# Kernel tuning notes

Measured on AMD Instinct MI355X. Metric: run time of the kernel, lower is better.

The kernel has to match this reference:

```python
import jax, jax.numpy as jnp
import numpy as np

C = 32        # channels after first 1x1 conv
HEADS = 4     # FuncSelfAttention heads ('channel' head split -> d = C // HEADS)


def setup_inputs() -> dict:
    key = jax.random.key(0)
    ks = jax.random.split(key, 8)
    B, H, W = 8, 512, 512
    s = 0.1
    return {
        "x": jax.random.normal(ks[0], (B, 1, H, W), jnp.float32),
        "n": 8,
        "m": 8,
        # Conv2d(1, C, kernel_size=1) == per-pixel linear 1->C
        "w1": jax.random.normal(ks[1], (C, 1), jnp.float32) * s,
        "b1": jax.random.normal(ks[2], (C,), jnp.float32) * s,
        # fused QKV projection over channels, bias=False
        "wqkv": jax.random.normal(ks[3], (3 * C, C), jnp.float32) * s,
        # output projection of the attention
        "wproj": jax.random.normal(ks[4], (C, C), jnp.float32) * s,
        "bproj": jax.random.normal(ks[5], (C,), jnp.float32) * s,
        # Conv2d(C, 1, kernel_size=1)
        "w2": jax.random.normal(ks[6], (1, C), jnp.float32) * s,
        "b2": jax.random.normal(ks[7], (1,), jnp.float32) * s,
    }


def reference(x, n, m, w1, b1, wqkv, wproj, bproj, w2, b2):
    B, _, H, W = x.shape
    d = C // HEADS
    hh, ww = H // n, W // m
    S, P = n * m, hh * ww  # subdomain tokens, quadrature points per token

    # 1x1 conv (pointwise linear over channel dim)
    h = jnp.einsum('oi,bihw->bohw', w1, x) + b1[None, :, None, None]

    # decompose2d: [B,C,H,W] -> [B, n*m, C, hh, ww] (flatten spatial per token)
    u = h.reshape(B, C, n, hh, m, ww).transpose(0, 2, 4, 1, 3, 5)
    u = u.reshape(B, S, C, P)

    # channel self-attention over subdomain functions
    qkv = jnp.einsum('oc,bscp->bsop', wqkv, u)          # [B,S,3C,P]
    q, k, v = jnp.split(qkv, 3, axis=2)
    q = q.reshape(B, S, HEADS, d, P)
    k = k.reshape(B, S, HEADS, d, P)
    v = v.reshape(B, S, HEADS, d, P)

    # L2 (quadrature-mean) inner product over points + head channels
    scale = 1.0 / (P * np.sqrt(d).astype(np.float32))
    scores = jnp.einsum('bihdp,bjhdp->bhij', q, k) * scale  # [B,H,S,S]
    attn = jax.nn.softmax(scores, axis=-1)
    o = jnp.einsum('bhij,bjhdp->bihdp', attn, v).reshape(B, S, C, P)
    o = jnp.einsum('oc,bscp->bsop', wproj, o) + bproj[None, None, :, None]

    # recompose2d: [B, n*m, C, hh, ww] -> [B, C, H, W]
    o = o.reshape(B, n, m, C, hh, ww).transpose(0, 3, 1, 4, 2, 5)
    o = o.reshape(B, C, H, W)

    # final 1x1 conv C -> 1
    out = jnp.einsum('oc,bchw->bohw', w2, o) + b2[None, :, None, None]
    return out
```

## Files before the change

### kernel.cpp

```cpp
#include <hip/hip_runtime.h>


#define CONST_OFF 0
#define SXP_OFF   16
#define W_OFF     (16 + 128*64)
#define PART_OFF  (W_OFF + 8*4096)

typedef __attribute__((ext_vector_type(8))) short bf16x8;
typedef __attribute__((ext_vector_type(4))) float f32x4;

__device__ __forceinline__ unsigned short f2bf(float f) {
    unsigned int u = __float_as_uint(f);
    u = (u + 0x7FFFu + ((u >> 16) & 1u)) >> 16;
    return (unsigned short)u;
}

__global__ __launch_bounds__(256) void k1_gram(const float* __restrict__ x,
                                               float* __restrict__ ws)
{
    __shared__ unsigned short xsb[64 * 272];
    int b = blockIdx.x >> 4, prg = blockIdx.x & 15;
    int t = threadIdx.x;
    const float* xb = x + (size_t)b * 262144;

    #pragma unroll
    for (int prl = 0; prl < 4; ++prl) {
        int pr = prg * 4 + prl;
        #pragma unroll
        for (int k = 0; k < 4; ++k) {
            int q = t + 256 * k;
            int tj = q >> 7, col4 = q & 127;
            float4 v = *(const float4*)(xb + (tj * 64 + pr) * 512 + col4 * 4);
            int token = tj * 8 + (col4 >> 4);
            ushort4 h;
            h.x = f2bf(v.x); h.y = f2bf(v.y); h.z = f2bf(v.z); h.w = f2bf(v.w);
            *(ushort4*)(&xsb[token * 272 + prl * 64 + (col4 & 15) * 4]) = h;
        }
    }
    __syncthreads();

    if (t < 64) {
        const uint4* p = (const uint4*)(&xsb[t * 272]);
        float s = 0.f;
        #pragma unroll
        for (int c = 0; c < 32; ++c) {
            uint4 u = p[c];
            s += __uint_as_float(u.x << 16) + __uint_as_float(u.x & 0xFFFF0000u)
               + __uint_as_float(u.y << 16) + __uint_as_float(u.y & 0xFFFF0000u)
               + __uint_as_float(u.z << 16) + __uint_as_float(u.z & 0xFFFF0000u)
               + __uint_as_float(u.w << 16) + __uint_as_float(u.w & 0xFFFF0000u);
        }
        ws[SXP_OFF + blockIdx.x * 64 + t] = s;
    }

    int w = t >> 6, lane = t & 63;
    int m = lane & 15, quad = lane >> 4;
    f32x4 acc[4];
    #pragma unroll
    for (int jq = 0; jq < 4; ++jq) acc[jq] = (f32x4){0.f, 0.f, 0.f, 0.f};

    #pragma unroll
    for (int s = 0; s < 8; ++s) {
        int kb = s * 32 + quad * 8;
        bf16x8 a = *(const bf16x8*)(&xsb[(w * 16 + m) * 272 + kb]);
        #pragma unroll
        for (int jq = 0; jq < 4; ++jq) {
            bf16x8 bb = *(const bf16x8*)(&xsb[(jq * 16 + m) * 272 + kb]);
            acc[jq] = __builtin_amdgcn_mfma_f32_16x16x32_bf16(a, bb, acc[jq],
                                                              0, 0, 0);
        }
    }

    float* part = ws + PART_OFF + (size_t)blockIdx.x * 4096;
    #pragma unroll
    for (int jq = 0; jq < 4; ++jq)
        #pragma unroll
        for (int r = 0; r < 4; ++r)
            part[(w * 16 + quad * 4 + r) * 64 + jq * 16 + m] = acc[jq][r];
}

__global__ __launch_bounds__(1024) void k2_attn(
    const float* __restrict__ w1, const float* __restrict__ b1,
    const float* __restrict__ wqkv, const float* __restrict__ wproj,
    const float* __restrict__ bproj, const float* __restrict__ w2,
    const float* __restrict__ b2, float* __restrict__ ws)
{
    __shared__ float arow[96], crow[96], pvec[32];
    __shared__ float cst[16];
    __shared__ float G_s[64 * 65];
    __shared__ float sxp_s[16][64];
    __shared__ float sx_s[64];
    __shared__ float coef_s[4][64];
    __shared__ float m_s[4][64];
    int b = blockIdx.x, t = threadIdx.x;

    if (t < 96) {
        float sa = 0.f, sc = 0.f;
        for (int c = 0; c < 32; ++c) {
            float w = wqkv[t * 32 + c];
            sa += w * w1[c];
            sc += w * b1[c];
        }
        arow[t] = sa; crow[t] = sc;
    } else if (t < 128) {
        int c = t - 96;
        float s = 0.f;
        for (int oc = 0; oc < 32; ++oc) s += w2[oc] * wproj[oc * 32 + c];
        pvec[c] = s;
    }

    {
        const float* p0 = ws + PART_OFF + (size_t)(b * 16) * 4096 + t;
        float a0 = 0.f, a1 = 0.f, a2 = 0.f, a3 = 0.f;
        #pragma unroll
        for (int r = 0; r < 16; ++r) {
            const float* pr = p0 + (size_t)r * 4096;
            a0 += pr[0]; a1 += pr[1024]; a2 += pr[2048]; a3 += pr[3072];
        }
        int e0 = t;
        G_s[(e0 >> 6) * 65 + (e0 & 63)] = a0;
        int e1 = t + 1024;
        G_s[(e1 >> 6) * 65 + (e1 & 63)] = a1;
        int e2 = t + 2048;
        G_s[(e2 >> 6) * 65 + (e2 & 63)] = a2;
        int e3 = t + 3072;
        G_s[(e3 >> 6) * 65 + (e3 & 63)] = a3;
    }

    {
        int j = t & 63, rg = t >> 6;
        sxp_s[rg][j] = ws[SXP_OFF + (b * 16 + rg) * 64 + j];
    }
    __syncthreads();
    if (t < 64) {
        float s = 0.f;
        #pragma unroll
        for (int r = 0; r < 16; ++r) s += sxp_s[r][t];
        sx_s[t] = s;
    }

    const float scale = 1.0f / (4096.0f * 2.8284271247461903f);
    if (t >= 64 && t < 68) {
        int h = t - 64;
        float A = 0.f, Bk = 0.f, g = 0.f;
        #pragma unroll
        for (int dd = 0; dd < 8; ++dd) {
            int o = h * 8 + dd;
            A  += arow[o] * arow[32 + o];
            Bk += crow[o] * arow[32 + o];
            g  += pvec[o] * arow[64 + o];
        }
        cst[h]     = A * scale;
        cst[4 + h] = Bk * scale;
        cst[8 + h] = g;
    } else if (t == 68) {
        float c0 = b2[0];
        for (int c = 0; c < 32; ++c)  c0 += pvec[c] * crow[64 + c];
        for (int oc = 0; oc < 32; ++oc) c0 += w2[oc] * bproj[oc];
        cst[12] = c0;
    }
    __syncthreads();

    if (t < 256) {
        int h = t >> 6, i = t & 63;
        float A  = cst[h];
        float Bk = cst[4 + h];
        float g  = cst[8 + h];
        float m = -1e30f;
        for (int j = 0; j < 64; ++j) {
            float s = A * G_s[i * 65 + j] + Bk * sx_s[j];
            m = fmaxf(m, s);
        }
        float Z = 0.f;
        for (int j = 0; j < 64; ++j) {
            float s = A * G_s[i * 65 + j] + Bk * sx_s[j];
            Z += __expf(s - m);
        }
        coef_s[h][i] = g / Z;
        m_s[h][i]    = m;
    }
    __syncthreads();

    {
        float A0 = cst[0], A1 = cst[1], A2 = cst[2], A3 = cst[3];
        float B0 = cst[4], B1 = cst[5], B2 = cst[6], B3 = cst[7];
        #pragma unroll
        for (int k = 0; k < 4; ++k) {
            int e = t + 1024 * k;
            int i = e >> 6, j = e & 63;
            float G  = G_s[i * 65 + j];
            float sx = sx_s[j];
            float w =
                coef_s[0][i] * __expf(A0 * G + B0 * sx - m_s[0][i]) +
                coef_s[1][i] * __expf(A1 * G + B1 * sx - m_s[1][i]) +
                coef_s[2][i] * __expf(A2 * G + B2 * sx - m_s[2][i]) +
                coef_s[3][i] * __expf(A3 * G + B3 * sx - m_s[3][i]);
            ws[W_OFF + b * 4096 + e] = w;
        }
    }
    if (b == 0 && t == 0) ws[CONST_OFF + 12] = cst[12];
}

__global__ __launch_bounds__(256) void k3_apply(const float* __restrict__ x,
                                                const float* __restrict__ ws,
                                                float* __restrict__ out)
{
    __shared__ unsigned short xt[64 * 72];
    __shared__ unsigned short wsm[64 * 72];
    int b = blockIdx.x >> 6, pr = blockIdx.x & 63;
    int t = threadIdx.x;
    const float* xb = x + (size_t)b * 262144;

    #pragma unroll
    for (int k = 0; k < 4; ++k) {
        int q = t + 256 * k;
        int j = q >> 4, c4 = q & 15;
        int ti = j >> 3, tk = j & 7;
        float4 v = *(const float4*)(xb + (ti * 64 + pr) * 512 + tk * 64 + c4 * 4);
        xt[(4 * c4 + 0) * 72 + j] = f2bf(v.x);
        xt[(4 * c4 + 1) * 72 + j] = f2bf(v.y);
        xt[(4 * c4 + 2) * 72 + j] = f2bf(v.z);
        xt[(4 * c4 + 3) * 72 + j] = f2bf(v.w);
        int i = q >> 4, j4 = q & 15;
        float4 wv = *(const float4*)(ws + W_OFF + b * 4096 + q * 4);
        ushort4 h;
        h.x = f2bf(wv.x); h.y = f2bf(wv.y); h.z = f2bf(wv.z); h.w = f2bf(wv.w);
        *(ushort4*)(&wsm[i * 72 + j4 * 4]) = h;
    }
    __syncthreads();

    int w = t >> 6, lane = t & 63;
    int m = lane & 15, quad = lane >> 4;
    f32x4 acc[4];
    #pragma unroll
    for (int jq = 0; jq < 4; ++jq) acc[jq] = (f32x4){0.f, 0.f, 0.f, 0.f};

    #pragma unroll
    for (int s = 0; s < 2; ++s) {
        int kb = s * 32 + quad * 8;
        bf16x8 a = *(const bf16x8*)(&wsm[(w * 16 + m) * 72 + kb]);
        #pragma unroll
        for (int jq = 0; jq < 4; ++jq) {
            bf16x8 bv = *(const bf16x8*)(&xt[(jq * 16 + m) * 72 + kb]);
            acc[jq] = __builtin_amdgcn_mfma_f32_16x16x32_bf16(a, bv, acc[jq],
                                                              0, 0, 0);
        }
    }

    float c0 = ws[CONST_OFF + 12];
    float* ob = out + (size_t)b * 262144;
    #pragma unroll
    for (int jq = 0; jq < 4; ++jq)
        #pragma unroll
        for (int r = 0; r < 4; ++r) {
            int i = w * 16 + quad * 4 + r;
            int c = jq * 16 + m;
            int ti = i >> 3, tk = i & 7;
            ob[(ti * 64 + pr) * 512 + tk * 64 + c] = acc[jq][r] + c0;
        }
}

extern "C" void kernel_launch(void* const* d_in, const int* in_sizes, int n_in,
                              void* d_out, int out_size, void* d_ws, size_t ws_size,
                              hipStream_t stream) {
    const float* x     = (const float*)d_in[0];
    const float* w1    = (const float*)d_in[3];
    const float* b1    = (const float*)d_in[4];
    const float* wqkv  = (const float*)d_in[5];
    const float* wproj = (const float*)d_in[6];
    const float* bproj = (const float*)d_in[7];
    const float* w2    = (const float*)d_in[8];
    const float* b2    = (const float*)d_in[9];
    float* out = (float*)d_out;
    float* ws  = (float*)d_ws;

    k1_gram<<<128, 256, 0, stream>>>(x, ws);
    k2_attn<<<8, 1024, 0, stream>>>(w1, b1, wqkv, wproj, bproj, w2, b2, ws);
    k3_apply<<<512, 256, 0, stream>>>(x, ws, out);
}
```

Measured before the change: 90.67 us.

## Split attention kernel across row groups and store mixing weights as bf16

The attention kernel now runs 64 blocks of 256 threads instead of 8 blocks of 1024. Each block reduces and processes only 8 rows of the 64x64 Gram matrix for one batch, which spreads the work over more compute units. Each block still recomputes the small weight-derived constants redundantly. The mixing-weight matrix is converted to bf16 inside the attention kernel, halving that workspace traffic, and the apply kernel loads it directly with 16-byte copies instead of converting from fp32.

```diff
diff --git a/kernel.cpp b/kernel.cpp
--- a/kernel.cpp
+++ b/kernel.cpp
@@ -3,8 +3,8 @@
 
 #define CONST_OFF 0
 #define SXP_OFF   16
-#define W_OFF     (16 + 128*64)
-#define PART_OFF  (W_OFF + 8*4096)
+#define WB_OFF    (16 + 128*64)
+#define PART_OFF  (WB_OFF + 8*2048)
 
 typedef __attribute__((ext_vector_type(8))) short bf16x8;
 typedef __attribute__((ext_vector_type(4))) float f32x4;
@@ -79,7 +79,7 @@
             part[(w * 16 + quad * 4 + r) * 64 + jq * 16 + m] = acc[jq][r];
 }
 
-__global__ __launch_bounds__(1024) void k2_attn(
+__global__ __launch_bounds__(256) void k2_attn(
     const float* __restrict__ w1, const float* __restrict__ b1,
     const float* __restrict__ wqkv, const float* __restrict__ wproj,
     const float* __restrict__ bproj, const float* __restrict__ w2,
@@ -87,12 +87,13 @@
 {
     __shared__ float arow[96], crow[96], pvec[32];
     __shared__ float cst[16];
-    __shared__ float G_s[64 * 65];
-    __shared__ float sxp_s[16][64];
+    __shared__ float G_s[8 * 65];
+    __shared__ float sxp_s[4][64];
     __shared__ float sx_s[64];
-    __shared__ float coef_s[4][64];
-    __shared__ float m_s[4][64];
-    int b = blockIdx.x, t = threadIdx.x;
+    __shared__ float coef_s[4][8];
+    __shared__ float m_s[4][8];
+    int b = blockIdx.x >> 3, rg = blockIdx.x & 7;
+    int t = threadIdx.x;
 
     if (t < 96) {
         float sa = 0.f, sc = 0.f;
@@ -110,34 +111,28 @@
     }
 
     {
-        const float* p0 = ws + PART_OFF + (size_t)(b * 16) * 4096 + t;
-        float a0 = 0.f, a1 = 0.f, a2 = 0.f, a3 = 0.f;
+        const float* p0 = ws + PART_OFF + (size_t)(b * 16) * 4096 + rg * 512;
+        float a0 = 0.f, a1 = 0.f;
         #pragma unroll
         for (int r = 0; r < 16; ++r) {
             const float* pr = p0 + (size_t)r * 4096;
-            a0 += pr[0]; a1 += pr[1024]; a2 += pr[2048]; a3 += pr[3072];
-        }
-        int e0 = t;
-        G_s[(e0 >> 6) * 65 + (e0 & 63)] = a0;
-        int e1 = t + 1024;
-        G_s[(e1 >> 6) * 65 + (e1 & 63)] = a1;
-        int e2 = t + 2048;
-        G_s[(e2 >> 6) * 65 + (e2 & 63)] = a2;
-        int e3 = t + 3072;
-        G_s[(e3 >> 6) * 65 + (e3 & 63)] = a3;
-    }
-
-    {
-        int j = t & 63, rg = t >> 6;
-        sxp_s[rg][j] = ws[SXP_OFF + (b * 16 + rg) * 64 + j];
-    }
-    __syncthreads();
-    if (t < 64) {
+            a0 += pr[t]; a1 += pr[t + 256];
+        }
+        int e0 = t;          G_s[(e0 >> 6) * 65 + (e0 & 63)] = a0;
+        int e1 = t + 256;    G_s[(e1 >> 6) * 65 + (e1 & 63)] = a1;
+    }
+
+    {
+        int j = t & 63, r4 = t >> 6;
         float s = 0.f;
         #pragma unroll
-        for (int r = 0; r < 16; ++r) s += sxp_s[r][t];
-        sx_s[t] = s;
-    }
+        for (int k = 0; k < 4; ++k)
+            s += ws[SXP_OFF + (b * 16 + r4 * 4 + k) * 64 + j];
+        sxp_s[r4][j] = s;
+    }
+    __syncthreads();
+    if (t < 64)
+        sx_s[t] = sxp_s[0][t] + sxp_s[1][t] + sxp_s[2][t] + sxp_s[3][t];
 
     const float scale = 1.0f / (4096.0f * 2.8284271247461903f);
     if (t >= 64 && t < 68) {
@@ -161,44 +156,46 @@
     }
     __syncthreads();
 
-    if (t < 256) {
-        int h = t >> 6, i = t & 63;
+    if (t < 32) {
+        int h = t >> 3, il = t & 7;
         float A  = cst[h];
         float Bk = cst[4 + h];
         float g  = cst[8 + h];
         float m = -1e30f;
         for (int j = 0; j < 64; ++j) {
-            float s = A * G_s[i * 65 + j] + Bk * sx_s[j];
+            float s = A * G_s[il * 65 + j] + Bk * sx_s[j];
             m = fmaxf(m, s);
         }
         float Z = 0.f;
         for (int j = 0; j < 64; ++j) {
-            float s = A * G_s[i * 65 + j] + Bk * sx_s[j];
+            float s = A * G_s[il * 65 + j] + Bk * sx_s[j];
             Z += __expf(s - m);
         }
-        coef_s[h][i] = g / Z;
-        m_s[h][i]    = m;
+        coef_s[h][il] = g / Z;
+        m_s[h][il]    = m;
     }
     __syncthreads();
 
     {
         float A0 = cst[0], A1 = cst[1], A2 = cst[2], A3 = cst[3];
         float B0 = cst[4], B1 = cst[5], B2 = cst[6], B3 = cst[7];
-        #pragma unroll
-        for (int k = 0; k < 4; ++k) {
-            int e = t + 1024 * k;
-            int i = e >> 6, j = e & 63;
-            float G  = G_s[i * 65 + j];
+        unsigned short* wout =
+            (unsigned short*)(ws + WB_OFF) + b * 4096 + rg * 512;
+        #pragma unroll
+        for (int k = 0; k < 2; ++k) {
+            int e = t + 256 * k;
+            int il = e >> 6, j = e & 63;
+            float G  = G_s[il * 65 + j];
             float sx = sx_s[j];
             float w =
-                coef_s[0][i] * __expf(A0 * G + B0 * sx - m_s[0][i]) +
-                coef_s[1][i] * __expf(A1 * G + B1 * sx - m_s[1][i]) +
-                coef_s[2][i] * __expf(A2 * G + B2 * sx - m_s[2][i]) +
-                coef_s[3][i] * __expf(A3 * G + B3 * sx - m_s[3][i]);
-            ws[W_OFF + b * 4096 + e] = w;
-        }
-    }
-    if (b == 0 && t == 0) ws[CONST_OFF + 12] = cst[12];
+                coef_s[0][il] * __expf(A0 * G + B0 * sx - m_s[0][il]) +
+                coef_s[1][il] * __expf(A1 * G + B1 * sx - m_s[1][il]) +
+                coef_s[2][il] * __expf(A2 * G + B2 * sx - m_s[2][il]) +
+                coef_s[3][il] * __expf(A3 * G + B3 * sx - m_s[3][il]);
+            wout[e] = f2bf(w);
+        }
+    }
+    if (b == 0 && rg == 0 && t == 68) ws[CONST_OFF + 12] = cst[12];
 }
 
 __global__ __launch_bounds__(256) void k3_apply(const float* __restrict__ x,
@@ -221,11 +218,16 @@
         xt[(4 * c4 + 1) * 72 + j] = f2bf(v.y);
         xt[(4 * c4 + 2) * 72 + j] = f2bf(v.z);
         xt[(4 * c4 + 3) * 72 + j] = f2bf(v.w);
-        int i = q >> 4, j4 = q & 15;
-        float4 wv = *(const float4*)(ws + W_OFF + b * 4096 + q * 4);
-        ushort4 h;
-        h.x = f2bf(wv.x); h.y = f2bf(wv.y); h.z = f2bf(wv.z); h.w = f2bf(wv.w);
-        *(ushort4*)(&wsm[i * 72 + j4 * 4]) = h;
+    }
+    {
+        const uint4* wb = (const uint4*)((const unsigned short*)(ws + WB_OFF)
+                                         + b * 4096);
+        #pragma unroll
+        for (int k = 0; k < 2; ++k) {
+            int q = t + 256 * k;
+            int i = q >> 3, j8 = q & 7;
+            *(uint4*)(&wsm[i * 72 + j8 * 8]) = wb[q];
+        }
     }
     __syncthreads();
 
@@ -275,6 +277,6 @@
     float* ws  = (float*)d_ws;
 
     k1_gram<<<128, 256, 0, stream>>>(x, ws);
-    k2_attn<<<8, 1024, 0, stream>>>(w1, b1, wqkv, wproj, bproj, w2, b2, ws);
+    k2_attn<<<64, 256, 0, stream>>>(w1, b1, wqkv, wproj, bproj, w2, b2, ws);
     k3_apply<<<512, 256, 0, stream>>>(x, ws, out);
 }
```

Measured after the change: 89.72 us. About the same (-1.1%).
